# Kernel optimization log

Hardware: AMD Instinct MI355X
Metric: run time of the kernel (lower is better)

## Reference

```python
import jax, jax.numpy as jnp
import numpy as np

N, R, E = 100000, 3, 500000
IN_F, HID_F, OUT_F = 128, 128, 32


def setup_inputs() -> dict:
    key = jax.random.key(0)
    ks = jax.random.split(key, 12)
    inp = {
        "x": jax.random.normal(ks[0], (N, IN_F), dtype=jnp.float32),
        "src": jax.random.randint(ks[1], (R, E), 0, N, dtype=jnp.int32),
        "dst": jax.random.randint(ks[2], (R, E), 0, N, dtype=jnp.int32),
        # per-relation weights for the 4 layers (Glorot-ish scale)
        "W0": jax.random.normal(ks[3], (R, IN_F, HID_F), dtype=jnp.float32) / np.sqrt(IN_F),
        "b0": jnp.zeros((R, HID_F), dtype=jnp.float32),
        "W1": jax.random.normal(ks[4], (R, HID_F, HID_F), dtype=jnp.float32) / np.sqrt(HID_F),
        "b1": jnp.zeros((R, HID_F), dtype=jnp.float32),
        "W2": jax.random.normal(ks[5], (R, HID_F, HID_F), dtype=jnp.float32) / np.sqrt(HID_F),
        "b2": jnp.zeros((R, HID_F), dtype=jnp.float32),
        "W3": jax.random.normal(ks[6], (R, HID_F, OUT_F), dtype=jnp.float32) / np.sqrt(HID_F),
        "b3": jnp.zeros((R, OUT_F), dtype=jnp.float32),
    }
    return inp


def _degree_norms(src, dst, n_nodes):
    # DGL GraphConv norm='both': clamp degree to >=1, use deg^-1/2
    ones = jnp.ones(src.shape[1], dtype=jnp.float32)
    dout = jax.vmap(lambda s: jax.ops.segment_sum(ones, s, num_segments=n_nodes))(src)
    din = jax.vmap(lambda d: jax.ops.segment_sum(ones, d, num_segments=n_nodes))(dst)
    return jnp.clip(dout, 1.0) ** -0.5, jnp.clip(din, 1.0) ** -0.5  # [R, N] each


def _hetero_layer(h, W, b, src, dst, dout_is, din_is, relu):
    # per-relation GraphConv (norm='both'), HeteroGraphConv aggregate='sum'
    n = h.shape[0]
    out = None
    for r in range(W.shape[0]):
        hs = h * dout_is[r][:, None]                          # [N, d] scale src
        msg = hs[src[r]]                                       # [E, d] gather
        agg = jax.ops.segment_sum(msg, dst[r], num_segments=n) # [N, d] scatter-add
        agg = agg * din_is[r][:, None]
        o = agg @ W[r] + b[r]
        if relu:
            o = jax.nn.relu(o)  # activation inside GraphConv, before cross-rel sum
        out = o if out is None else out + o
    return out


def reference(x, src, dst, W0, b0, W1, b1, W2, b2, W3, b3):
    dout_is, din_is = _degree_norms(src, dst, x.shape[0])
    h = _hetero_layer(x, W0, b0, src, dst, dout_is, din_is, relu=True)
    h = _hetero_layer(h, W1, b1, src, dst, dout_is, din_is, relu=True)
    h = _hetero_layer(h, W2, b2, src, dst, dout_is, din_is, relu=True)
    h = _hetero_layer(h, W3, b3, src, dst, dout_is, din_is, relu=False)
    return h  # [N, OUT_F]
```

## Files before the change

### kernel.cpp

```cpp
#include <hip/hip_runtime.h>
#include <cstdint>
#include <cstddef>

#define NN 100000
#define RR 3
#define EE 500000
#define RN 300000
#define RE 1500000
#define KK 384
#define CAP 32

typedef unsigned short u16;
typedef unsigned int   u32;
typedef __attribute__((ext_vector_type(8))) short bhalf8;
typedef __attribute__((ext_vector_type(4))) float f32x4;

static inline int cdiv_h(int a, int b){ return (a+b-1)/b; }

__device__ __forceinline__ float bf_lo(u32 v){ union{u32 u; float f;} c; c.u = v<<16; return c.f; }
__device__ __forceinline__ float bf_hi(u32 v){ union{u32 u; float f;} c; c.u = v & 0xffff0000u; return c.f; }
__device__ __forceinline__ u16 f2bf(float f){
  union{float f; u32 u;} c; c.f = f;
  u32 r = (c.u + 0x7FFFu + ((c.u >> 16) & 1u)) >> 16;
  return (u16)r;
}
__device__ __forceinline__ u32 pk2(float a, float b){ return (u32)f2bf(a) | ((u32)f2bf(b)<<16); }

__global__ __launch_bounds__(256) void k_init(int* __restrict__ cursor, int* __restrict__ dout_cnt){
  int i = blockIdx.x*256 + threadIdx.x;
  if (i < RN){ cursor[i] = i*CAP; dout_cnt[i] = 0; }
}

__global__ __launch_bounds__(256) void k_pre1f(const int* __restrict__ src, const int* __restrict__ dst,
    int* __restrict__ cursor, int* __restrict__ dout_cnt, int* __restrict__ edge_src,
    const float* __restrict__ x, u16* __restrict__ xb,
    const float* __restrict__ W0, const float* __restrict__ W1, const float* __restrict__ W2,
    const float* __restrict__ W3, u16* __restrict__ Wtb, u16* __restrict__ Wt3b){
  int b = blockIdx.x, t = threadIdx.x;
  if (b < 5860){
    int i = b*256 + t;
    if (i < RE){
      int r = i / EE;
      int s = src[i], d = dst[i];
      atomicAdd(&dout_cnt[r*NN + s], 1);
      int idx = r*NN + d;
      int pos = atomicAdd(&cursor[idx], 1);
      if (pos < idx*CAP + CAP) edge_src[pos] = s;
    }
  } else if (b < 12110){
    int i = (b-5860)*256 + t;
    if (i < NN*128/8){
      float4 v0 = ((const float4*)x)[i*2];
      float4 v1 = ((const float4*)x)[i*2+1];
      uint4 o;
      o.x = pk2(v0.x, v0.y); o.y = pk2(v0.z, v0.w);
      o.z = pk2(v1.x, v1.y); o.w = pk2(v1.z, v1.w);
      ((uint4*)xb)[i] = o;
    }
  } else if (b < 12686){
    int gid = (b-12110)*256 + t;
    if (gid < 3*3*16384){
      int l = gid / 49152; int rem = gid - l*49152;
      int r = rem >> 14; int rem2 = rem & 16383;
      int k = rem2 >> 7; int n = rem2 & 127;
      const float* Wl = (l==0) ? W0 : (l==1) ? W1 : W2;
      Wtb[((size_t)(l*3+r))*16384 + (size_t)n*128 + k] = f2bf(Wl[rem]);
    }
  } else {
    int gid = (b-12686)*256 + t;
    if (gid < 3*4096){
      int r = gid >> 12; int rem = gid & 4095;
      int k = rem >> 5; int n = rem & 31;
      Wt3b[(size_t)(r*32+n)*128 + k] = f2bf(W3[gid]);
    }
  }
}

__global__ __launch_bounds__(256) void k_norms(const int* __restrict__ dout_cnt, float* __restrict__ dout_is){
  int i = blockIdx.x*256 + threadIdx.x;
  if (i < RN){
    int dc = dout_cnt[i] > 1 ? dout_cnt[i] : 1;
    dout_is[i] = rsqrtf((float)dc);
  }
}

__global__ __launch_bounds__(256) void k_agg_bf(const u16* __restrict__ h, u16* __restrict__ AGG,
    const int* __restrict__ cursor, const int* __restrict__ edge_src,
    const float* __restrict__ dout_is){
  int w = (blockIdx.x*256 + threadIdx.x) >> 6;
  if (w >= RN) return;
  int l = threadIdx.x & 63;
  int q = l >> 4, k = l & 15;
  int r = w / NN;
  int n = w - r*NN;
  int s0 = w*CAP;
  int s1 = cursor[w];
  if (s1 > s0 + CAP) s1 = s0 + CAP;
  const float* __restrict__ dis = dout_is + r*NN;
  const uint4* __restrict__ h4 = (const uint4*)h;
  float a[8] = {0.f,0.f,0.f,0.f,0.f,0.f,0.f,0.f};
  for (int p = s0 + q; p < s1; p += 4){
    int s = edge_src[p];
    float wg = dis[s];
    uint4 v = h4[(size_t)s*16 + k];
    a[0] += wg*bf_lo(v.x); a[1] += wg*bf_hi(v.x);
    a[2] += wg*bf_lo(v.y); a[3] += wg*bf_hi(v.y);
    a[4] += wg*bf_lo(v.z); a[5] += wg*bf_hi(v.z);
    a[6] += wg*bf_lo(v.w); a[7] += wg*bf_hi(v.w);
  }
  #pragma unroll
  for (int i=0;i<8;i++){
    a[i] += __shfl_xor(a[i], 16);
    a[i] += __shfl_xor(a[i], 32);
  }
  if (q == 0){
    int cnt = s1 - s0;
    float di = rsqrtf((float)(cnt > 1 ? cnt : 1));
    uint4 o;
    o.x = pk2(a[0]*di, a[1]*di);
    o.y = pk2(a[2]*di, a[3]*di);
    o.z = pk2(a[4]*di, a[5]*di);
    o.w = pk2(a[6]*di, a[7]*di);
    ((uint4*)AGG)[(size_t)n*48 + r*16 + k] = o;
  }
}

__global__ __launch_bounds__(256) void k_mm_relu(const u16* __restrict__ A, const u16* __restrict__ Wt,
    const float* __restrict__ bias, u16* __restrict__ out){
  __shared__ __align__(16) u16 As[128*128];
  __shared__ __align__(16) u16 Bs[128*128];
  int t = threadIdx.x;
  int l = t & 63, w = t >> 6;
  int wr = w >> 1, wc = w & 1;
  int row0 = blockIdx.x * 128;
  int tr = t >> 4, tc = t & 15;
  int swz = tr & 7;

  f32x4 res[4][4];
  #pragma unroll
  for (int m=0;m<4;m++)
    #pragma unroll
    for (int n=0;n<4;n++) res[m][n] = (f32x4){0.f,0.f,0.f,0.f};

  for (int r=0; r<RR; r++){
    uint4 ra[8], rb[8];
    #pragma unroll
    for (int it=0; it<8; ++it){
      int grow = row0 + it*16 + tr;
      if (grow > NN-1) grow = NN-1;
      ra[it] = *(const uint4*)&A[(size_t)grow*KK + r*128 + tc*8];
      rb[it] = *(const uint4*)&Wt[(size_t)r*16384 + (size_t)(it*16 + tr)*128 + tc*8];
    }
    __syncthreads();
    #pragma unroll
    for (int it=0; it<8; ++it){
      int rho = it*16 + tr;
      int ch = (tc ^ swz) * 8;
      *(uint4*)&As[rho*128 + ch] = ra[it];
      *(uint4*)&Bs[rho*128 + ch] = rb[it];
    }
    __syncthreads();

    f32x4 acc[4][4];
    #pragma unroll
    for (int m=0;m<4;m++)
      #pragma unroll
      for (int n=0;n<4;n++) acc[m][n] = (f32x4){0.f,0.f,0.f,0.f};

    #pragma unroll
    for (int kk=0; kk<4; ++kk){
      bhalf8 af[4], bf[4];
      #pragma unroll
      for (int m=0;m<4;m++){
        int rho = wr*64 + m*16 + (l&15);
        int ch = (kk*4 + (l>>4)) ^ (l&7);
        af[m] = *(const bhalf8*)&As[rho*128 + ch*8];
      }
      #pragma unroll
      for (int n=0;n<4;n++){
        int rho = wc*64 + n*16 + (l&15);
        int ch = (kk*4 + (l>>4)) ^ (l&7);
        bf[n] = *(const bhalf8*)&Bs[rho*128 + ch*8];
      }
      #pragma unroll
      for (int m=0;m<4;m++)
        #pragma unroll
        for (int n=0;n<4;n++)
          acc[m][n] = __builtin_amdgcn_mfma_f32_16x16x32_bf16(af[m], bf[n], acc[m][n], 0, 0, 0);
    }

    #pragma unroll
    for (int n=0;n<4;n++){
      int col = wc*64 + n*16 + (l&15);
      float bb = bias[r*128 + col];
      #pragma unroll
      for (int m=0;m<4;m++)
        #pragma unroll
        for (int i=0;i<4;i++){
          float v = acc[m][n][i] + bb;
          res[m][n][i] += v > 0.f ? v : 0.f;
        }
    }
  }

  #pragma unroll
  for (int m=0;m<4;m++)
    #pragma unroll
    for (int i=0;i<4;i++){
      int grow = row0 + wr*64 + m*16 + (l>>4)*4 + i;
      if (grow < NN){
        #pragma unroll
        for (int n=0;n<4;n++)
          out[(size_t)grow*128 + wc*64 + n*16 + (l&15)] = f2bf(res[m][n][i]);
      }
    }
}

__global__ __launch_bounds__(256) void k_mm_y(const u16* __restrict__ A, const u16* __restrict__ Wt3,
    u16* __restrict__ y){
  __shared__ __align__(16) u16 As[128*128];
  __shared__ __align__(16) u16 Bs[96*128];
  int t = threadIdx.x;
  int l = t & 63, w = t >> 6;
  int wr = w & 1, wc = w >> 1;
  int row0 = blockIdx.x * 128;
  int tr = t >> 4, tc = t & 15;
  int swz = tr & 7;

  uint4 ra[8], rb[6];
  #pragma unroll
  for (int it=0; it<8; ++it){
    int grow = row0 + it*16 + tr;
    if (grow > NN-1) grow = NN-1;
    ra[it] = *(const uint4*)&A[(size_t)grow*128 + tc*8];
  }
  #pragma unroll
  for (int it=0; it<6; ++it)
    rb[it] = *(const uint4*)&Wt3[(size_t)(it*16 + tr)*128 + tc*8];
  #pragma unroll
  for (int it=0; it<8; ++it)
    *(uint4*)&As[(it*16+tr)*128 + ((tc ^ swz)*8)] = ra[it];
  #pragma unroll
  for (int it=0; it<6; ++it)
    *(uint4*)&Bs[(it*16+tr)*128 + ((tc ^ swz)*8)] = rb[it];
  __syncthreads();

  f32x4 acc[4][3];
  #pragma unroll
  for (int m=0;m<4;m++)
    #pragma unroll
    for (int n=0;n<3;n++) acc[m][n] = (f32x4){0.f,0.f,0.f,0.f};

  #pragma unroll
  for (int kk=0; kk<4; ++kk){
    bhalf8 af[4], bf[3];
    #pragma unroll
    for (int m=0;m<4;m++){
      int rho = wr*64 + m*16 + (l&15);
      int ch = (kk*4 + (l>>4)) ^ (l&7);
      af[m] = *(const bhalf8*)&As[rho*128 + ch*8];
    }
    #pragma unroll
    for (int n=0;n<3;n++){
      int rho = wc*48 + n*16 + (l&15);
      int ch = (kk*4 + (l>>4)) ^ (l&7);
      bf[n] = *(const bhalf8*)&Bs[rho*128 + ch*8];
    }
    #pragma unroll
    for (int m=0;m<4;m++)
      #pragma unroll
      for (int n=0;n<3;n++)
        acc[m][n] = __builtin_amdgcn_mfma_f32_16x16x32_bf16(af[m], bf[n], acc[m][n], 0, 0, 0);
  }

  #pragma unroll
  for (int m=0;m<4;m++)
    #pragma unroll
    for (int i=0;i<4;i++){
      int grow = row0 + wr*64 + m*16 + (l>>4)*4 + i;
      if (grow < NN){
        #pragma unroll
        for (int n=0;n<3;n++)
          y[(size_t)grow*96 + wc*48 + n*16 + (l&15)] = f2bf(acc[m][n][i]);
      }
    }
}

__global__ __launch_bounds__(256) void k_agg_out(const u16* __restrict__ y, float* __restrict__ out,
    const int* __restrict__ cursor, const int* __restrict__ edge_src,
    const float* __restrict__ dout_is, const float* __restrict__ b3){
  int n = (blockIdx.x*256 + threadIdx.x) >> 6;
  if (n >= NN) return;
  int l = threadIdx.x & 63;
  int g = l >> 3, k = l & 7;
  float res[4];
  #pragma unroll
  for (int i=0;i<4;i++) res[i] = b3[4*k+i] + b3[32+4*k+i] + b3[64+4*k+i];
  const uint2* __restrict__ y2 = (const uint2*)y;
  for (int r=0; r<RR; r++){
    int w = r*NN + n;
    int s0 = w*CAP;
    int s1 = cursor[w];
    if (s1 > s0 + CAP) s1 = s0 + CAP;
    const float* __restrict__ dis = dout_is + r*NN;
    float a[4] = {0.f,0.f,0.f,0.f};
    for (int p = s0 + g; p < s1; p += 8){
      int s = edge_src[p];
      float wg = dis[s];
      uint2 v = y2[(size_t)s*24 + r*8 + k];
      a[0] += wg*bf_lo(v.x); a[1] += wg*bf_hi(v.x);
      a[2] += wg*bf_lo(v.y); a[3] += wg*bf_hi(v.y);
    }
    #pragma unroll
    for (int i=0;i<4;i++){
      a[i] += __shfl_xor(a[i], 8);
      a[i] += __shfl_xor(a[i], 16);
      a[i] += __shfl_xor(a[i], 32);
    }
    int cnt = s1 - s0;
    float di = rsqrtf((float)(cnt>1?cnt:1));
    #pragma unroll
    for (int i=0;i<4;i++) res[i] += di*a[i];
  }
  if (g == 0)
    ((float4*)out)[(size_t)n*8 + k] = make_float4(res[0],res[1],res[2],res[3]);
}


extern "C" void kernel_launch(void* const* d_in, const int* in_sizes, int n_in,
                              void* d_out, int out_size, void* d_ws, size_t ws_size,
                              hipStream_t stream){
  const float* x   = (const float*)d_in[0];
  const int*   src = (const int*)d_in[1];
  const int*   dst = (const int*)d_in[2];
  const float* W0  = (const float*)d_in[3]; const float* b0 = (const float*)d_in[4];
  const float* W1  = (const float*)d_in[5]; const float* b1 = (const float*)d_in[6];
  const float* W2  = (const float*)d_in[7]; const float* b2 = (const float*)d_in[8];
  const float* W3  = (const float*)d_in[9]; const float* b3 = (const float*)d_in[10];
  float* out = (float*)d_out;

  char* p = (char*)d_ws;
  auto alloc = [&](size_t bytes)->char*{
    char* q = p; p += (bytes + 255) & ~(size_t)255; return q;
  };
  int*   cursor   = (int*)  alloc(RN*4);
  int*   dout_cnt = (int*)  alloc(RN*4);
  float* dout_is  = (float*)alloc(RN*4);
  u16*   Wtb      = (u16*)  alloc((size_t)3*3*16384*2);
  u16*   Wt3b     = (u16*)  alloc((size_t)3*32*128*2);
  u16*   AGG      = (u16*)  alloc((size_t)NN*KK*2);
  u16*   bufA     = (u16*)  alloc((size_t)NN*128*2);
  u16*   bufB     = (u16*)  alloc((size_t)NN*128*2);
  int*   edge_src = (int*)  alloc((size_t)RN*CAP*4);
  u16*   y        = AGG;

  k_init <<<cdiv_h(RN,256),256,0,stream>>>(cursor, dout_cnt);
  k_pre1f<<<12734,256,0,stream>>>(src, dst, cursor, dout_cnt, edge_src,
                                  x, bufB, W0,W1,W2,W3, Wtb, Wt3b);
  k_norms<<<cdiv_h(RN,256),256,0,stream>>>(dout_cnt, dout_is);

  int agg_blocks = cdiv_h(RN,4);
  int mm_blocks  = cdiv_h(NN,128);

  k_agg_bf<<<agg_blocks,256,0,stream>>>(bufB, AGG, cursor, edge_src, dout_is);
  k_mm_relu<<<mm_blocks,256,0,stream>>>(AGG, Wtb, b0, bufA);
  k_agg_bf<<<agg_blocks,256,0,stream>>>(bufA, AGG, cursor, edge_src, dout_is);
  k_mm_relu<<<mm_blocks,256,0,stream>>>(AGG, Wtb + 3*16384, b1, bufB);
  k_agg_bf<<<agg_blocks,256,0,stream>>>(bufB, AGG, cursor, edge_src, dout_is);
  k_mm_relu<<<mm_blocks,256,0,stream>>>(AGG, Wtb + 6*16384, b2, bufA);
  k_mm_y<<<mm_blocks,256,0,stream>>>(bufA, Wt3b, y);
  k_agg_out<<<cdiv_h(NN,4),256,0,stream>>>(y, out, cursor, edge_src, dout_is, b3);
}
```

Measured before the change: 776.3 us.

## Drop norm kernel, prefetch next-relation tiles in matmul, add nontemporal hints, relayout y

Removes the separate k_norms launch and the dout_is buffer. The aggregation kernels now compute each source node's inverse-sqrt degree inline from the integer counts. The relu matmul issues the next relation's A-tile global loads before the current relation's MFMA work, so load latency overlaps compute. Nontemporal load and store hints are added to streaming buffers, and the layer-3 output y is stored relation-major so the final aggregation reads contiguous 64-byte rows. The trade-off is an extra rsqrt per edge and a per-edge load of a count instead of a precomputed float.

Measured after the change: 656.7 us, median of 2. 1.18x faster.

```diff
diff --git a/kernel.cpp b/kernel.cpp
--- a/kernel.cpp
+++ b/kernel.cpp
@@ -14,6 +14,8 @@
 typedef unsigned int   u32;
 typedef __attribute__((ext_vector_type(8))) short bhalf8;
 typedef __attribute__((ext_vector_type(4))) float f32x4;
+typedef __attribute__((ext_vector_type(4))) unsigned int u32x4;
+typedef __attribute__((ext_vector_type(2))) unsigned int u32x2;
 
 static inline int cdiv_h(int a, int b){ return (a+b-1)/b; }
 
@@ -25,6 +27,7 @@
   return (u16)r;
 }
 __device__ __forceinline__ u32 pk2(float a, float b){ return (u32)f2bf(a) | ((u32)f2bf(b)<<16); }
+__device__ __forceinline__ float invdeg(int c){ return rsqrtf((float)(c > 1 ? c : 1)); }
 
 __global__ __launch_bounds__(256) void k_init(int* __restrict__ cursor, int* __restrict__ dout_cnt){
   int i = blockIdx.x*256 + threadIdx.x;
@@ -52,10 +55,10 @@
     if (i < NN*128/8){
       float4 v0 = ((const float4*)x)[i*2];
       float4 v1 = ((const float4*)x)[i*2+1];
-      uint4 o;
+      u32x4 o;
       o.x = pk2(v0.x, v0.y); o.y = pk2(v0.z, v0.w);
       o.z = pk2(v1.x, v1.y); o.w = pk2(v1.z, v1.w);
-      ((uint4*)xb)[i] = o;
+      __builtin_nontemporal_store(o, &((u32x4*)xb)[i]);
     }
   } else if (b < 12686){
     int gid = (b-12110)*256 + t;
@@ -64,29 +67,23 @@
       int r = rem >> 14; int rem2 = rem & 16383;
       int k = rem2 >> 7; int n = rem2 & 127;
       const float* Wl = (l==0) ? W0 : (l==1) ? W1 : W2;
-      Wtb[((size_t)(l*3+r))*16384 + (size_t)n*128 + k] = f2bf(Wl[rem]);
+      __builtin_nontemporal_store(f2bf(Wl[rem]),
+          &Wtb[((size_t)(l*3+r))*16384 + (size_t)n*128 + k]);
     }
   } else {
     int gid = (b-12686)*256 + t;
     if (gid < 3*4096){
       int r = gid >> 12; int rem = gid & 4095;
       int k = rem >> 5; int n = rem & 31;
-      Wt3b[(size_t)(r*32+n)*128 + k] = f2bf(W3[gid]);
-    }
-  }
-}
-
-__global__ __launch_bounds__(256) void k_norms(const int* __restrict__ dout_cnt, float* __restrict__ dout_is){
-  int i = blockIdx.x*256 + threadIdx.x;
-  if (i < RN){
-    int dc = dout_cnt[i] > 1 ? dout_cnt[i] : 1;
-    dout_is[i] = rsqrtf((float)dc);
+      __builtin_nontemporal_store(f2bf(W3[gid]),
+          &Wt3b[(size_t)(r*32+n)*128 + k]);
+    }
   }
 }
 
 __global__ __launch_bounds__(256) void k_agg_bf(const u16* __restrict__ h, u16* __restrict__ AGG,
     const int* __restrict__ cursor, const int* __restrict__ edge_src,
-    const float* __restrict__ dout_is){
+    const int* __restrict__ dout_cnt){
   int w = (blockIdx.x*256 + threadIdx.x) >> 6;
   if (w >= RN) return;
   int l = threadIdx.x & 63;
@@ -96,13 +93,13 @@
   int s0 = w*CAP;
   int s1 = cursor[w];
   if (s1 > s0 + CAP) s1 = s0 + CAP;
-  const float* __restrict__ dis = dout_is + r*NN;
-  const uint4* __restrict__ h4 = (const uint4*)h;
+  const int* __restrict__ dct = dout_cnt + r*NN;
+  const u32x4* __restrict__ h4 = (const u32x4*)h;
   float a[8] = {0.f,0.f,0.f,0.f,0.f,0.f,0.f,0.f};
   for (int p = s0 + q; p < s1; p += 4){
     int s = edge_src[p];
-    float wg = dis[s];
-    uint4 v = h4[(size_t)s*16 + k];
+    float wg = invdeg(dct[s]);
+    u32x4 v = h4[(size_t)s*16 + k];
     a[0] += wg*bf_lo(v.x); a[1] += wg*bf_hi(v.x);
     a[2] += wg*bf_lo(v.y); a[3] += wg*bf_hi(v.y);
     a[4] += wg*bf_lo(v.z); a[5] += wg*bf_hi(v.z);
@@ -114,14 +111,13 @@
     a[i] += __shfl_xor(a[i], 32);
   }
   if (q == 0){
-    int cnt = s1 - s0;
-    float di = rsqrtf((float)(cnt > 1 ? cnt : 1));
-    uint4 o;
+    float di = invdeg(s1 - s0);
+    u32x4 o;
     o.x = pk2(a[0]*di, a[1]*di);
     o.y = pk2(a[2]*di, a[3]*di);
     o.z = pk2(a[4]*di, a[5]*di);
     o.w = pk2(a[6]*di, a[7]*di);
-    ((uint4*)AGG)[(size_t)n*48 + r*16 + k] = o;
+    __builtin_nontemporal_store(o, &((u32x4*)AGG)[(size_t)n*48 + r*16 + k]);
   }
 }
 
@@ -136,30 +132,37 @@
   int tr = t >> 4, tc = t & 15;
   int swz = tr & 7;
 
+  int grow[8];
+  #pragma unroll
+  for (int it=0; it<8; ++it){
+    int gr = row0 + it*16 + tr;
+    grow[it] = gr > NN-1 ? NN-1 : gr;
+  }
+
   f32x4 res[4][4];
   #pragma unroll
   for (int m=0;m<4;m++)
     #pragma unroll
     for (int n=0;n<4;n++) res[m][n] = (f32x4){0.f,0.f,0.f,0.f};
 
+  u32x4 ra[8];
+  #pragma unroll
+  for (int it=0; it<8; ++it){
+    ra[it] = __builtin_nontemporal_load((const u32x4*)&A[(size_t)grow[it]*KK + tc*8]);
+    u32x4 rb = *(const u32x4*)&Wt[(size_t)(it*16 + tr)*128 + tc*8];
+    *(u32x4*)&Bs[(it*16+tr)*128 + ((tc ^ swz)*8)] = rb;
+  }
+  #pragma unroll
+  for (int it=0; it<8; ++it)
+    *(u32x4*)&As[(it*16+tr)*128 + ((tc ^ swz)*8)] = ra[it];
+  __syncthreads();
+
   for (int r=0; r<RR; r++){
-    uint4 ra[8], rb[8];
-    #pragma unroll
-    for (int it=0; it<8; ++it){
-      int grow = row0 + it*16 + tr;
-      if (grow > NN-1) grow = NN-1;
-      ra[it] = *(const uint4*)&A[(size_t)grow*KK + r*128 + tc*8];
-      rb[it] = *(const uint4*)&Wt[(size_t)r*16384 + (size_t)(it*16 + tr)*128 + tc*8];
-    }
-    __syncthreads();
-    #pragma unroll
-    for (int it=0; it<8; ++it){
-      int rho = it*16 + tr;
-      int ch = (tc ^ swz) * 8;
-      *(uint4*)&As[rho*128 + ch] = ra[it];
-      *(uint4*)&Bs[rho*128 + ch] = rb[it];
-    }
-    __syncthreads();
+    if (r+1 < RR){
+      #pragma unroll
+      for (int it=0; it<8; ++it)
+        ra[it] = __builtin_nontemporal_load((const u32x4*)&A[(size_t)grow[it]*KK + (r+1)*128 + tc*8]);
+    }
 
     f32x4 acc[4][4];
     #pragma unroll
@@ -201,17 +204,28 @@
           res[m][n][i] += v > 0.f ? v : 0.f;
         }
     }
+
+    if (r+1 < RR){
+      __syncthreads();
+      #pragma unroll
+      for (int it=0; it<8; ++it){
+        u32x4 rb = *(const u32x4*)&Wt[(size_t)(r+1)*16384 + (size_t)(it*16 + tr)*128 + tc*8];
+        *(u32x4*)&As[(it*16+tr)*128 + ((tc ^ swz)*8)] = ra[it];
+        *(u32x4*)&Bs[(it*16+tr)*128 + ((tc ^ swz)*8)] = rb;
+      }
+      __syncthreads();
+    }
   }
 
   #pragma unroll
   for (int m=0;m<4;m++)
     #pragma unroll
     for (int i=0;i<4;i++){
-      int grow = row0 + wr*64 + m*16 + (l>>4)*4 + i;
-      if (grow < NN){
+      int gr = row0 + wr*64 + m*16 + (l>>4)*4 + i;
+      if (gr < NN){
         #pragma unroll
         for (int n=0;n<4;n++)
-          out[(size_t)grow*128 + wc*64 + n*16 + (l&15)] = f2bf(res[m][n][i]);
+          out[(size_t)gr*128 + wc*64 + n*16 + (l&15)] = f2bf(res[m][n][i]);
       }
     }
 }
@@ -227,22 +241,22 @@
   int tr = t >> 4, tc = t & 15;
   int swz = tr & 7;
 
-  uint4 ra[8], rb[6];
+  u32x4 ra[8], rb[6];
   #pragma unroll
   for (int it=0; it<8; ++it){
     int grow = row0 + it*16 + tr;
     if (grow > NN-1) grow = NN-1;
-    ra[it] = *(const uint4*)&A[(size_t)grow*128 + tc*8];
+    ra[it] = __builtin_nontemporal_load((const u32x4*)&A[(size_t)grow*128 + tc*8]);
   }
   #pragma unroll
   for (int it=0; it<6; ++it)
-    rb[it] = *(const uint4*)&Wt3[(size_t)(it*16 + tr)*128 + tc*8];
+    rb[it] = *(const u32x4*)&Wt3[(size_t)(it*16 + tr)*128 + tc*8];
   #pragma unroll
   for (int it=0; it<8; ++it)
-    *(uint4*)&As[(it*16+tr)*128 + ((tc ^ swz)*8)] = ra[it];
+    *(u32x4*)&As[(it*16+tr)*128 + ((tc ^ swz)*8)] = ra[it];
   #pragma unroll
   for (int it=0; it<6; ++it)
-    *(uint4*)&Bs[(it*16+tr)*128 + ((tc ^ swz)*8)] = rb[it];
+    *(u32x4*)&Bs[(it*16+tr)*128 + ((tc ^ swz)*8)] = rb[it];
   __syncthreads();
 
   f32x4 acc[4][3];
@@ -277,18 +291,20 @@
   for (int m=0;m<4;m++)
     #pragma unroll
     for (int i=0;i<4;i++){
-      int grow = row0 + wr*64 + m*16 + (l>>4)*4 + i;
-      if (grow < NN){
+      int gr = row0 + wr*64 + m*16 + (l>>4)*4 + i;
+      if (gr < NN){
         #pragma unroll
-        for (int n=0;n<3;n++)
-          y[(size_t)grow*96 + wc*48 + n*16 + (l&15)] = f2bf(acc[m][n][i]);
+        for (int n=0;n<3;n++){
+          int c = wc*48 + n*16 + (l&15);
+          y[((size_t)(c>>5)*NN + gr)*32 + (c&31)] = f2bf(acc[m][n][i]);
+        }
       }
     }
 }
 
 __global__ __launch_bounds__(256) void k_agg_out(const u16* __restrict__ y, float* __restrict__ out,
     const int* __restrict__ cursor, const int* __restrict__ edge_src,
-    const float* __restrict__ dout_is, const float* __restrict__ b3){
+    const int* __restrict__ dout_cnt, const float* __restrict__ b3){
   int n = (blockIdx.x*256 + threadIdx.x) >> 6;
   if (n >= NN) return;
   int l = threadIdx.x & 63;
@@ -296,18 +312,18 @@
   float res[4];
   #pragma unroll
   for (int i=0;i<4;i++) res[i] = b3[4*k+i] + b3[32+4*k+i] + b3[64+4*k+i];
-  const uint2* __restrict__ y2 = (const uint2*)y;
+  const u32x2* __restrict__ y2 = (const u32x2*)y;
   for (int r=0; r<RR; r++){
     int w = r*NN + n;
     int s0 = w*CAP;
     int s1 = cursor[w];
     if (s1 > s0 + CAP) s1 = s0 + CAP;
-    const float* __restrict__ dis = dout_is + r*NN;
+    const int* __restrict__ dct = dout_cnt + r*NN;
     float a[4] = {0.f,0.f,0.f,0.f};
     for (int p = s0 + g; p < s1; p += 8){
       int s = edge_src[p];
-      float wg = dis[s];
-      uint2 v = y2[(size_t)s*24 + r*8 + k];
+      float wg = invdeg(dct[s]);
+      u32x2 v = y2[((size_t)r*NN + s)*8 + k];
       a[0] += wg*bf_lo(v.x); a[1] += wg*bf_hi(v.x);
       a[2] += wg*bf_lo(v.y); a[3] += wg*bf_hi(v.y);
     }
@@ -317,8 +333,7 @@
       a[i] += __shfl_xor(a[i], 16);
       a[i] += __shfl_xor(a[i], 32);
     }
-    int cnt = s1 - s0;
-    float di = rsqrtf((float)(cnt>1?cnt:1));
+    float di = invdeg(s1 - s0);
     #pragma unroll
     for (int i=0;i<4;i++) res[i] += di*a[i];
   }
@@ -345,7 +360,6 @@
   };
   int*   cursor   = (int*)  alloc(RN*4);
   int*   dout_cnt = (int*)  alloc(RN*4);
-  float* dout_is  = (float*)alloc(RN*4);
   u16*   Wtb      = (u16*)  alloc((size_t)3*3*16384*2);
   u16*   Wt3b     = (u16*)  alloc((size_t)3*32*128*2);
   u16*   AGG      = (u16*)  alloc((size_t)NN*KK*2);
@@ -357,17 +371,16 @@
   k_init <<<cdiv_h(RN,256),256,0,stream>>>(cursor, dout_cnt);
   k_pre1f<<<12734,256,0,stream>>>(src, dst, cursor, dout_cnt, edge_src,
                                   x, bufB, W0,W1,W2,W3, Wtb, Wt3b);
-  k_norms<<<cdiv_h(RN,256),256,0,stream>>>(dout_cnt, dout_is);
 
   int agg_blocks = cdiv_h(RN,4);
   int mm_blocks  = cdiv_h(NN,128);
 
-  k_agg_bf<<<agg_blocks,256,0,stream>>>(bufB, AGG, cursor, edge_src, dout_is);
+  k_agg_bf<<<agg_blocks,256,0,stream>>>(bufB, AGG, cursor, edge_src, dout_cnt);
   k_mm_relu<<<mm_blocks,256,0,stream>>>(AGG, Wtb, b0, bufA);
-  k_agg_bf<<<agg_blocks,256,0,stream>>>(bufA, AGG, cursor, edge_src, dout_is);
+  k_agg_bf<<<agg_blocks,256,0,stream>>>(bufA, AGG, cursor, edge_src, dout_cnt);
   k_mm_relu<<<mm_blocks,256,0,stream>>>(AGG, Wtb + 3*16384, b1, bufB);
-  k_agg_bf<<<agg_blocks,256,0,stream>>>(bufB, AGG, cursor, edge_src, dout_is);
+  k_agg_bf<<<agg_blocks,256,0,stream>>>(bufB, AGG, cursor, edge_src, dout_cnt);
   k_mm_relu<<<mm_blocks,256,0,stream>>>(AGG, Wtb + 6*16384, b2, bufA);
   k_mm_y<<<mm_blocks,256,0,stream>>>(bufA, Wt3b, y);
-  k_agg_out<<<cdiv_h(NN,4),256,0,stream>>>(y, out, cursor, edge_src, dout_is, b3);
-}
+  k_agg_out<<<cdiv_h(NN,4),256,0,stream>>>(y, out, cursor, edge_src, dout_cnt, b3);
+}
```
